# Optimization experiments

Measured on AMD Instinct MI355X. Metric: run time of the kernel, lower is better.

Reference implementation:

```python
import jax, jax.numpy as jnp
import numpy as np

CAP_FACTOR = 1.25


def _moe_top1(x, wg, w1, b1, w2, b2):
    """Top-1 switch MoE with capacity-based token dropping.
    x: [T, d]; wg: [d, E]; w1: [E, d, f]; b1: [E, f]; w2: [E, f, d]; b2: [E, d].
    """
    T, d = x.shape
    E = wg.shape[1]
    cap = int(CAP_FACTOR * T / E)
    probs = jax.nn.softmax(x @ wg, axis=-1)            # [T, E]
    idx = jnp.argmax(probs, axis=-1)                   # [T] expert assignment
    gate = jnp.max(probs, axis=-1)                     # [T] gate prob
    oh = jax.nn.one_hot(idx, E, dtype=jnp.int32)       # [T, E]
    # position of each token within its expert's buffer
    pos = (jnp.cumsum(oh, axis=0) * oh).sum(-1) - 1    # [T]
    keep = pos < cap                                   # drop tokens over capacity
    pos_w = jnp.where(keep, pos, cap)                  # dropped -> overflow slot
    # dispatch: scatter tokens into per-expert buffers [E, cap+1, d]
    buf = jnp.zeros((E, cap + 1, d), dtype=x.dtype).at[idx, pos_w].set(x)
    buf = buf[:, :cap]                                 # slice off overflow slot
    # grouped expert FFN
    h = jax.nn.relu(jnp.einsum('ecd,edf->ecf', buf, w1) + b1[:, None, :])
    eo = jnp.einsum('ecf,efd->ecd', h, w2) + b2[:, None, :]
    # combine: gather each token's expert output, scale by gate prob, zero dropped
    pos_g = jnp.minimum(pos_w, cap - 1)
    out = eo[idx, pos_g] * (gate * keep.astype(x.dtype))[:, None]
    return out


def setup_inputs():
    key = jax.random.key(0)
    ks = jax.random.split(key, 12)
    B, S, d, dff, E1, E2 = 8, 2048, 1024, 4096, 8, 16
    s = lambda fan: np.float32(1.0 / np.sqrt(fan))
    return dict(
        x=jax.random.normal(ks[0], (B, S, d), jnp.float32),
        y=jax.random.randint(ks[1], (B,), 0, d),
        wg1=jax.random.normal(ks[2], (d, E1), jnp.float32) * s(d),
        w1a=jax.random.normal(ks[3], (E1, d, dff), jnp.float32) * s(d),
        b1a=jnp.zeros((E1, dff), jnp.float32),
        w2a=jax.random.normal(ks[4], (E1, dff, d), jnp.float32) * s(dff),
        b2a=jnp.zeros((E1, d), jnp.float32),
        wg2=jax.random.normal(ks[5], (d, E2), jnp.float32) * s(d),
        w1b=jax.random.normal(ks[6], (E2, d, dff), jnp.float32) * s(d),
        b1b=jnp.zeros((E2, dff), jnp.float32),
        w2b=jax.random.normal(ks[7], (E2, dff, d), jnp.float32) * s(dff),
        b2b=jnp.zeros((E2, d), jnp.float32),
    )


def reference(x, y, wg1, w1a, b1a, w2a, b2a, wg2, w1b, b1b, w2b, b2b):
    B, S, d = x.shape
    xf = x.reshape(B * S, d)
    m1 = _moe_top1(xf, wg1, w1a, b1a, w2a, b2a)        # moe1(x)
    m2 = _moe_top1(m1, wg2, w1b, b1b, w2b, b2b)        # moe2(moe_out)
    resid = x + m2.reshape(B, S, d)                    # residual add
    sent = resid.mean(axis=1)                          # [B, d] mean-pool -> logits
    logp = jax.nn.log_softmax(sent, axis=-1)
    return -logp[jnp.arange(B), y].mean()              # cross-entropy loss
```

## Files before the change

### kernel.cpp

```cpp
#include <hip/hip_runtime.h>
#include <hip/hip_bf16.h>
#include <cstdint>
#include <cstddef>

#define B_    8
#define S_    2048
#define D_    1024
#define DFF_  4096
#define E1_   8
#define E2_   16
#define T_    (B_*S_)
#define CAP1_ 2560
#define CAP2_ 1280
#define EC_   20480

typedef __bf16 bf16x8 __attribute__((ext_vector_type(8)));
typedef float  f32x4  __attribute__((ext_vector_type(4)));

__device__ __forceinline__ unsigned short f2bf(float x) {
  return __builtin_bit_cast(unsigned short, (__bf16)x);
}

template<int E>
__global__ __launch_bounds__(256)
void gate_kernel(const float* __restrict__ X, const float* __restrict__ WG,
                 int* __restrict__ idxO, float* __restrict__ gateO) {
  const int lane = threadIdx.x & 63;
  const int wv   = threadIdx.x >> 6;
  const int t    = blockIdx.x * 4 + wv;
  const float* xr = X + (size_t)t * D_;
  float acc[E];
#pragma unroll
  for (int e = 0; e < E; ++e) acc[e] = 0.f;
#pragma unroll
  for (int i = 0; i < 4; ++i) {
    float4 xv = *(const float4*)(xr + i * 256 + lane * 4);
    int kb = i * 256 + lane * 4;
#pragma unroll
    for (int j = 0; j < 4; ++j) {
      float xs = (&xv.x)[j];
      const float* wr = WG + (size_t)(kb + j) * E;
#pragma unroll
      for (int e = 0; e < E; ++e) acc[e] += xs * wr[e];
    }
  }
#pragma unroll
  for (int e = 0; e < E; ++e) {
    float v = acc[e];
#pragma unroll
    for (int s = 32; s >= 1; s >>= 1) v += __shfl_xor(v, s, 64);
    acc[e] = v;
  }
  if (lane == 0) {
    float mx = acc[0]; int mi = 0;
#pragma unroll
    for (int e = 1; e < E; ++e) if (acc[e] > mx) { mx = acc[e]; mi = e; }
    float s = 0.f;
#pragma unroll
    for (int e = 0; e < E; ++e) s += expf(acc[e] - mx);
    idxO[t]  = mi;
    gateO[t] = 1.0f / s;
  }
}

__global__ __launch_bounds__(1024)
void scan_kernel(const int* __restrict__ idx, int E, int cap,
                 int* __restrict__ pos, int* __restrict__ kept) {
  __shared__ int cnt[16][17];
  __shared__ int gbase[16];
  const int tid = threadIdx.x;
  const int w = tid >> 6, lane = tid & 63;
  if (tid < E) gbase[tid] = 0;
  __syncthreads();
  const unsigned long long lt = (lane == 63) ? 0xFFFFFFFFFFFFFFFFull >> 1
                                             : ((1ull << lane) - 1ull);
  for (int it = 0; it < T_ / 1024; ++it) {
    int t = it * 1024 + tid;
    int mi = idx[t];
    int rank = 0;
    for (int e = 0; e < E; ++e) {
      unsigned long long m = __ballot(mi == e);
      if (lane == 0) cnt[w][e] = __popcll(m);
      if (mi == e) rank = __popcll(m & lt);
    }
    __syncthreads();
    int off = 0;
    for (int w2 = 0; w2 < w; ++w2) off += cnt[w2][mi];
    pos[t] = gbase[mi] + off + rank;
    __syncthreads();
    if (tid < E) {
      int tot = 0;
      for (int w2 = 0; w2 < 16; ++w2) tot += cnt[w2][tid];
      gbase[tid] += tot;
    }
    __syncthreads();
  }
  if (tid < E) kept[tid] = min(gbase[tid], cap);
}

__global__ __launch_bounds__(64)
void scatter_kernel(const float* __restrict__ X, const int* __restrict__ idx,
                    const int* __restrict__ pos, int cap,
                    unsigned short* __restrict__ xbuf, int* __restrict__ tokmap,
                    float* __restrict__ mzero) {
  const int t = blockIdx.x;
  const int lane = threadIdx.x;
  const int p = pos[t];
  if (p < cap) {
    const size_t dst = ((size_t)idx[t] * cap + p) * D_;
    const float* xr = X + (size_t)t * D_;
#pragma unroll
    for (int i = 0; i < 4; ++i) {
      float4 v = *(const float4*)(xr + i * 256 + lane * 4);
      ushort4 o;
      o.x = f2bf(v.x); o.y = f2bf(v.y); o.z = f2bf(v.z); o.w = f2bf(v.w);
      *(ushort4*)(xbuf + dst + i * 256 + lane * 4) = o;
    }
    if (lane == 0) tokmap[(size_t)idx[t] * cap + p] = t;
  } else {
    float4 z = {0.f, 0.f, 0.f, 0.f};
    float* mr = mzero + (size_t)t * D_;
#pragma unroll
    for (int i = 0; i < 4; ++i) *(float4*)(mr + i * 256 + lane * 4) = z;
  }
}

__global__ __launch_bounds__(256)
void wtrans_kernel(const float* __restrict__ src, unsigned short* __restrict__ dst,
                   int K, int N) {
  __shared__ float t[64][65];
  const int tid = threadIdx.x;
  const size_t eo = (size_t)blockIdx.z * K * N;
  const int k0 = blockIdx.y * 64, n0 = blockIdx.x * 64;
  const float* s = src + eo + (size_t)k0 * N + n0;
  unsigned short* d = dst + eo + (size_t)n0 * K + k0;
#pragma unroll
  for (int i = 0; i < 4; ++i) {
    int k = i * 16 + (tid >> 4);
    int n4 = (tid & 15) * 4;
    float4 v = *(const float4*)(s + (size_t)k * N + n4);
    t[k][n4] = v.x; t[k][n4 + 1] = v.y; t[k][n4 + 2] = v.z; t[k][n4 + 3] = v.w;
  }
  __syncthreads();
#pragma unroll
  for (int i = 0; i < 4; ++i) {
    int n = i * 16 + (tid >> 4);
    int k4 = (tid & 15) * 4;
    ushort4 o;
    o.x = f2bf(t[k4][n]);     o.y = f2bf(t[k4 + 1][n]);
    o.z = f2bf(t[k4 + 2][n]); o.w = f2bf(t[k4 + 3][n]);
    *(ushort4*)(d + (size_t)n * K + k4) = o;
  }
}

#define STG(BASEPTR, H, KT, SLOT) do {                                          \
    const unsigned short* _s = (BASEPTR) + (size_t)((H) * 128) * K + (KT) + st_off; \
    __builtin_amdgcn_global_load_lds((const __attribute__((address_space(1))) void*)_s, \
        (__attribute__((address_space(3))) void*)(smem + (SLOT) + dst0), 16, 0, 0);   \
    __builtin_amdgcn_global_load_lds((const __attribute__((address_space(1))) void*)(_s + (size_t)64 * K), \
        (__attribute__((address_space(3))) void*)(smem + (SLOT) + 8192 + dst0), 16, 0, 0); \
  } while (0)

#define RDA(BUF, MH) do { _Pragma("unroll")                                     \
    for (int m_ = 0; m_ < 4; ++m_) {                                            \
      const char* _p = smem + (BUF) * 65536 + aslot + ((MH) * 4 + m_) * 2048;   \
      af[m_][0] = *(const bf16x8*)(_p + va);                                    \
      af[m_][1] = *(const bf16x8*)(_p + (va ^ 64)); } } while (0)

#define RDB01(BUF, DEST) do { _Pragma("unroll")                                 \
    for (int j_ = 0; j_ < 2; ++j_) {                                            \
      const char* _p = smem + (BUF) * 65536 + bslot + j_ * 2048;                \
      DEST[j_][0] = *(const bf16x8*)(_p + vb);                                  \
      DEST[j_][1] = *(const bf16x8*)(_p + (vb ^ 64)); } } while (0)

#define RDB23(BUF) do { _Pragma("unroll")                                       \
    for (int j_ = 0; j_ < 2; ++j_) {                                            \
      const char* _p = smem + (BUF) * 65536 + bslot + (2 + j_) * 2048;          \
      bfb[j_][0] = *(const bf16x8*)(_p + vb);                                   \
      bfb[j_][1] = *(const bf16x8*)(_p + (vb ^ 64)); } } while (0)

#define QUADN0(MH, BA) do {                                                     \
    __builtin_amdgcn_s_setprio(1);                                              \
    _Pragma("unroll") for (int m_ = 0; m_ < 4; ++m_)                            \
    _Pragma("unroll") for (int j_ = 0; j_ < 2; ++j_)                            \
    _Pragma("unroll") for (int k_ = 0; k_ < 2; ++k_)                            \
      acc[(MH) * 4 + m_][j_] = __builtin_amdgcn_mfma_f32_16x16x32_bf16(         \
          af[m_][k_], BA[j_][k_], acc[(MH) * 4 + m_][j_], 0, 0, 0);             \
    __builtin_amdgcn_s_setprio(0);                                              \
  } while (0)

#define QUADN1(MH) do {                                                         \
    __builtin_amdgcn_s_setprio(1);                                              \
    _Pragma("unroll") for (int m_ = 0; m_ < 4; ++m_)                            \
    _Pragma("unroll") for (int j_ = 0; j_ < 2; ++j_)                            \
    _Pragma("unroll") for (int k_ = 0; k_ < 2; ++k_)                            \
      acc[(MH) * 4 + m_][2 + j_] = __builtin_amdgcn_mfma_f32_16x16x32_bf16(     \
          af[m_][k_], bfb[j_][k_], acc[(MH) * 4 + m_][2 + j_], 0, 0, 0);        \
    __builtin_amdgcn_s_setprio(0);                                              \
  } while (0)

#define SB0   __builtin_amdgcn_sched_barrier(0)
#define BAR   __builtin_amdgcn_s_barrier()
#define VM6   do { asm volatile("s_waitcnt vmcnt(6)" ::: "memory"); SB0; } while (0)
#define VM8   do { asm volatile("s_waitcnt vmcnt(8)" ::: "memory"); SB0; } while (0)
#define VM0   do { asm volatile("s_waitcnt vmcnt(0)" ::: "memory"); SB0; } while (0)

template<int MODE>
__global__ __launch_bounds__(512, 2)
void moe_gemm(const unsigned short* __restrict__ A,
              const unsigned short* __restrict__ BT,
              const float* __restrict__ bias, int K, int N, int cap, int nbcnt,
              const int* __restrict__ kept,
              unsigned short* __restrict__ Hout, float* __restrict__ Mout,
              const int* __restrict__ tokmap, const float* __restrict__ gate) {
  __shared__ char smem[131072];
  const int tid  = threadIdx.x;
  const int lane = tid & 63;
  const int wv   = tid >> 6;
  const int wr   = wv >> 2;
  const int wc   = wv & 3;

  const int nwg = gridDim.x;
  const int wg  = (blockIdx.x & 7) * (nwg >> 3) + (blockIdx.x >> 3);
  const int per_grp = nbcnt * 4;
  const int grp = wg / per_grp;
  const int rem = wg - grp * per_grp;
  const int mb  = grp * 4 + (rem & 3);
  const int nb  = rem >> 2;

  const int e  = (mb * 256) / cap;
  const int r0 = mb * 256 - e * cap;
  const int kept_e = kept[e];
  if (r0 >= kept_e) return;
  const unsigned short* Ab = A + (size_t)(mb * 256) * K;
  const unsigned short* Bb = BT + ((size_t)e * N + (size_t)nb * 256) * K;

  f32x4 acc[8][4];
#pragma unroll
  for (int m = 0; m < 8; ++m)
#pragma unroll
    for (int n = 0; n < 4; ++n) acc[m][n] = (f32x4){0.f, 0.f, 0.f, 0.f};

  const int scol   = ((tid & 7) ^ ((tid >> 3) & 7)) * 8;
  const size_t st_off = (size_t)(tid >> 3) * K + scol;
  const int dst0   = tid * 16;

  const int r16 = lane & 15;
  const int g16 = (lane >> 4) * 16;
  const int swz = (r16 & 7) * 16;
  const int va  = r16 * 128 + (g16 ^ swz);
  const int vb  = (wc & 1) * 8192 + va;
  const int aslot = wr * 16384;
  const int bslot = 32768 + (wc >> 1) * 16384;
  bf16x8 af[4][2], bA0[2][2], bA1[2][2], bfb[2][2];


  STG(Ab, 0, 0, 0);
  STG(Bb, 0, 0, 32768);
  STG(Bb, 1, 0, 49152);
  STG(Ab, 1, 0, 16384);
  STG(Ab, 0, 64, 65536);
  STG(Bb, 0, 64, 98304);
  STG(Bb, 1, 64, 114688);
  STG(Ab, 1, 64, 81920);
  VM8; BAR;
  RDB01(0, bA0);

  const int NT = K >> 6;
  const int NI = K >> 7;
  for (int i = 0; i < NI; ++i) {
    const bool last = (i == NI - 1);
    const bool s2 = (2 * i + 2) < NT;
    const bool s3 = (2 * i + 3) < NT;
    const int kt1 = (2 * i + 1) << 6;
    const int kt2 = (2 * i + 2) << 6;
    const int kt3 = (2 * i + 3) << 6;

    RDA(0, 0);
    if (i > 0) STG(Ab, 1, kt1, 81920);
    BAR; QUADN0(0, bA0); BAR;
    RDB23(0);
    if (s2) STG(Ab, 0, kt2, 0);
    BAR; QUADN1(0); BAR;
    RDA(0, 1);
    if (s2) STG(Bb, 0, kt2, 32768);
    BAR; QUADN1(1); BAR;
    if (s2) STG(Bb, 1, kt2, 49152);
    if (last) { VM0; } else { VM6; }
    RDB01(1, bA1);
    BAR; QUADN0(1, bA0); BAR;
    RDA(1, 0);
    if (s2) STG(Ab, 1, kt2, 16384);
    BAR; QUADN0(0, bA1); BAR;
    RDB23(1);
    if (s3) STG(Ab, 0, kt3, 65536);
    BAR; QUADN1(0); BAR;
    RDA(1, 1);
    if (s3) STG(Bb, 0, kt3, 98304);
    BAR; QUADN1(1); BAR;
    if (s3) STG(Bb, 1, kt3, 114688);
    if (!last) { VM6; RDB01(0, bA0); }
    BAR; QUADN0(1, bA1); BAR;
  }

  const int rg = lane >> 4;
  float bv[4];
#pragma unroll
  for (int n = 0; n < 4; ++n)
    bv[n] = bias[(size_t)e * N + nb * 256 + wc * 64 + n * 16 + r16];

#pragma unroll
  for (int m = 0; m < 8; ++m) {
#pragma unroll
    for (int r = 0; r < 4; ++r) {
      const int lrow = wr * 128 + m * 16 + rg * 4 + r;
      if (MODE == 0) {
        unsigned short* orow = Hout + (size_t)(mb * 256 + lrow) * N + nb * 256;
#pragma unroll
        for (int n = 0; n < 4; ++n) {
          float v = acc[m][n][r] + bv[n];
          orow[wc * 64 + n * 16 + r16] = f2bf(fmaxf(v, 0.f));
        }
      } else {
        const int lr = r0 + lrow;
        if (lr < kept_e) {
          const int tok = tokmap[mb * 256 + lrow];
          const float gsc = gate[tok];
          float* orow = Mout + (size_t)tok * N + nb * 256;
#pragma unroll
          for (int n = 0; n < 4; ++n)
            orow[wc * 64 + n * 16 + r16] = (acc[m][n][r] + bv[n]) * gsc;
        }
      }
    }
  }
}

__global__ __launch_bounds__(256)
void reduce_kernel(const float* __restrict__ X, const float* __restrict__ M2,
                   float* __restrict__ sent) {
  const int c = blockIdx.x * 256 + threadIdx.x;
  const int b = blockIdx.z;
  const int s0 = blockIdx.y * 128;
  float a = 0.f;
  size_t base = ((size_t)b * S_ + s0) * D_ + c;
  for (int s = 0; s < 128; ++s) a += X[base + (size_t)s * D_] + M2[base + (size_t)s * D_];
  atomicAdd(&sent[b * D_ + c], a * (1.0f / (float)S_));
}

__global__ __launch_bounds__(64)
void loss_kernel(const float* __restrict__ sent, const int* __restrict__ y,
                 float* __restrict__ out) {
  const int lane = threadIdx.x;
  float total = 0.f;
  for (int b = 0; b < B_; ++b) {
    const float* s = sent + b * D_;
    float v[16];
    float mx = -1e30f;
#pragma unroll
    for (int i = 0; i < 16; ++i) { v[i] = s[lane + i * 64]; mx = fmaxf(mx, v[i]); }
#pragma unroll
    for (int sh = 32; sh >= 1; sh >>= 1) mx = fmaxf(mx, __shfl_xor(mx, sh, 64));
    float sm = 0.f;
#pragma unroll
    for (int i = 0; i < 16; ++i) sm += expf(v[i] - mx);
#pragma unroll
    for (int sh = 32; sh >= 1; sh >>= 1) sm += __shfl_xor(sm, sh, 64);
    total += logf(sm) + mx - s[y[b]];
  }
  if (lane == 0) out[0] = total * (1.0f / (float)B_);
}

extern "C" void kernel_launch(void* const* d_in, const int* in_sizes, int n_in,
                              void* d_out, int out_size, void* d_ws, size_t ws_size,
                              hipStream_t stream) {
  const float* x   = (const float*)d_in[0];
  const int*   y   = (const int*)d_in[1];
  const float* wg1 = (const float*)d_in[2];
  const float* w1a = (const float*)d_in[3];
  const float* b1a = (const float*)d_in[4];
  const float* w2a = (const float*)d_in[5];
  const float* b2a = (const float*)d_in[6];
  const float* wg2 = (const float*)d_in[7];
  const float* w1b = (const float*)d_in[8];
  const float* b1b = (const float*)d_in[9];
  const float* w2b = (const float*)d_in[10];
  const float* b2b = (const float*)d_in[11];
  float* out = (float*)d_out;
  (void)in_sizes; (void)n_in; (void)out_size; (void)ws_size;

  char* base = (char*)d_ws;
  size_t o = 0;
  auto alloc = [&](size_t bytes) { size_t r = o; o = (o + bytes + 255) & ~(size_t)255; return r; };
  int*   idx1    = (int*)  (base + alloc((size_t)T_ * 4));
  int*   pos1    = (int*)  (base + alloc((size_t)T_ * 4));
  float* gate1   = (float*)(base + alloc((size_t)T_ * 4));
  int*   idx2    = (int*)  (base + alloc((size_t)T_ * 4));
  int*   pos2    = (int*)  (base + alloc((size_t)T_ * 4));
  float* gate2   = (float*)(base + alloc((size_t)T_ * 4));
  int*   kept1   = (int*)  (base + alloc(64 * 4));
  int*   kept2   = (int*)  (base + alloc(64 * 4));
  int*   tokmap1 = (int*)  (base + alloc((size_t)EC_ * 4));
  int*   tokmap2 = (int*)  (base + alloc((size_t)EC_ * 4));
  float* sent    = (float*)(base + alloc((size_t)B_ * D_ * 4));
  float* m1      = (float*)(base + alloc((size_t)T_ * D_ * 4));
  unsigned short* xbuf = (unsigned short*)(base + alloc((size_t)EC_ * D_ * 2));
  unsigned short* h    = (unsigned short*)(base + alloc((size_t)EC_ * DFF_ * 2));
  unsigned short* wT   = (unsigned short*)(base + alloc((size_t)E2_ * D_ * DFF_ * 2));

  hipMemsetAsync(sent, 0, (size_t)B_ * D_ * 4, stream);

  gate_kernel<E1_><<<T_ / 4, 256, 0, stream>>>(x, wg1, idx1, gate1);
  scan_kernel<<<1, 1024, 0, stream>>>(idx1, E1_, CAP1_, pos1, kept1);
  scatter_kernel<<<T_, 64, 0, stream>>>(x, idx1, pos1, CAP1_, xbuf, tokmap1, m1);
  wtrans_kernel<<<dim3(DFF_ / 64, D_ / 64, E1_), 256, 0, stream>>>(w1a, wT, D_, DFF_);
  moe_gemm<0><<<(DFF_ / 256) * (EC_ / 256), 512, 0, stream>>>(
      xbuf, wT, b1a, D_, DFF_, CAP1_, DFF_ / 256, kept1, h, nullptr, nullptr, nullptr);
  wtrans_kernel<<<dim3(D_ / 64, DFF_ / 64, E1_), 256, 0, stream>>>(w2a, wT, DFF_, D_);
  moe_gemm<1><<<(D_ / 256) * (EC_ / 256), 512, 0, stream>>>(
      h, wT, b2a, DFF_, D_, CAP1_, D_ / 256, kept1, nullptr, m1, tokmap1, gate1);

  gate_kernel<E2_><<<T_ / 4, 256, 0, stream>>>(m1, wg2, idx2, gate2);
  scan_kernel<<<1, 1024, 0, stream>>>(idx2, E2_, CAP2_, pos2, kept2);
  scatter_kernel<<<T_, 64, 0, stream>>>(m1, idx2, pos2, CAP2_, xbuf, tokmap2, m1);
  wtrans_kernel<<<dim3(DFF_ / 64, D_ / 64, E2_), 256, 0, stream>>>(w1b, wT, D_, DFF_);
  moe_gemm<0><<<(DFF_ / 256) * (EC_ / 256), 512, 0, stream>>>(
      xbuf, wT, b1b, D_, DFF_, CAP2_, DFF_ / 256, kept2, h, nullptr, nullptr, nullptr);
  wtrans_kernel<<<dim3(D_ / 64, DFF_ / 64, E2_), 256, 0, stream>>>(w2b, wT, DFF_, D_);
  moe_gemm<1><<<(D_ / 256) * (EC_ / 256), 512, 0, stream>>>(
      h, wT, b2b, DFF_, D_, CAP2_, D_ / 256, kept2, nullptr, m1, tokmap2, gate2);

  reduce_kernel<<<dim3(D_ / 256, S_ / 128, B_), 256, 0, stream>>>(x, m1, sent);
  loss_kernel<<<1, 64, 0, stream>>>(sent, y, out);
}
```

Baseline: 1.293 ms.

## Split-K the second expert GEMM with atomic accumulation into output

The down-projection GEMM (K=4096, N=1024) launches only 320 tiles, which may underfill the GPU. The K dimension is split in half so twice as many workgroups run, and each half atomically adds its gated partial result into the output. The scatter kernel now zeroes every output row, including kept tokens, so the atomic adds start from zero. In exchange this adds atomic traffic, extra zeroing writes, and a nondeterministic float summation order.

Measured after the change: 1.426 ms. 1.1x slower.

```diff
diff --git a/kernel.cpp b/kernel.cpp
--- a/kernel.cpp
+++ b/kernel.cpp
@@ -106,20 +106,21 @@
   const int t = blockIdx.x;
   const int lane = threadIdx.x;
   const int p = pos[t];
+  const float* xr = X + (size_t)t * D_;
+  float* mr = mzero + (size_t)t * D_;
+  const float4 z = {0.f, 0.f, 0.f, 0.f};
   if (p < cap) {
     const size_t dst = ((size_t)idx[t] * cap + p) * D_;
-    const float* xr = X + (size_t)t * D_;
 #pragma unroll
     for (int i = 0; i < 4; ++i) {
       float4 v = *(const float4*)(xr + i * 256 + lane * 4);
       ushort4 o;
       o.x = f2bf(v.x); o.y = f2bf(v.y); o.z = f2bf(v.z); o.w = f2bf(v.w);
       *(ushort4*)(xbuf + dst + i * 256 + lane * 4) = o;
+      *(float4*)(mr + i * 256 + lane * 4) = z;
     }
     if (lane == 0) tokmap[(size_t)idx[t] * cap + p] = t;
   } else {
-    float4 z = {0.f, 0.f, 0.f, 0.f};
-    float* mr = mzero + (size_t)t * D_;
 #pragma unroll
     for (int i = 0; i < 4; ++i) *(float4*)(mr + i * 256 + lane * 4) = z;
   }
@@ -209,7 +210,8 @@
 __global__ __launch_bounds__(512, 2)
 void moe_gemm(const unsigned short* __restrict__ A,
               const unsigned short* __restrict__ BT,
-              const float* __restrict__ bias, int K, int N, int cap, int nbcnt,
+              const float* __restrict__ bias, int K, int Kloop, int N, int cap,
+              int nbcnt, int ntiles,
               const int* __restrict__ kept,
               unsigned short* __restrict__ Hout, float* __restrict__ Mout,
               const int* __restrict__ tokmap, const float* __restrict__ gate) {
@@ -220,8 +222,12 @@
   const int wr   = wv >> 2;
   const int wc   = wv & 3;
 
-  const int nwg = gridDim.x;
-  const int wg  = (blockIdx.x & 7) * (nwg >> 3) + (blockIdx.x >> 3);
+  const int bid   = blockIdx.x;
+  const int khalf = (bid >= ntiles) ? 1 : 0;
+  const int lbid  = bid - khalf * ntiles;
+  const int koff  = khalf * Kloop;
+  const bool split = (Kloop != K);
+  const int wg  = (lbid & 7) * (ntiles >> 3) + (lbid >> 3);
   const int per_grp = nbcnt * 4;
   const int grp = wg / per_grp;
   const int rem = wg - grp * per_grp;
@@ -232,8 +238,8 @@
   const int r0 = mb * 256 - e * cap;
   const int kept_e = kept[e];
   if (r0 >= kept_e) return;
-  const unsigned short* Ab = A + (size_t)(mb * 256) * K;
-  const unsigned short* Bb = BT + ((size_t)e * N + (size_t)nb * 256) * K;
+  const unsigned short* Ab = A + (size_t)(mb * 256) * K + koff;
+  const unsigned short* Bb = BT + ((size_t)e * N + (size_t)nb * 256) * K + koff;
 
   f32x4 acc[8][4];
 #pragma unroll
@@ -266,8 +272,8 @@
   VM8; BAR;
   RDB01(0, bA0);
 
-  const int NT = K >> 6;
-  const int NI = K >> 7;
+  const int NT = Kloop >> 6;
+  const int NI = Kloop >> 7;
   for (int i = 0; i < NI; ++i) {
     const bool last = (i == NI - 1);
     const bool s2 = (2 * i + 2) < NT;
@@ -327,9 +333,17 @@
           const int tok = tokmap[mb * 256 + lrow];
           const float gsc = gate[tok];
           float* orow = Mout + (size_t)tok * N + nb * 256;
-#pragma unroll
-          for (int n = 0; n < 4; ++n)
-            orow[wc * 64 + n * 16 + r16] = (acc[m][n][r] + bv[n]) * gsc;
+          if (split) {
+#pragma unroll
+            for (int n = 0; n < 4; ++n) {
+              float v = acc[m][n][r] + (koff == 0 ? bv[n] : 0.f);
+              atomicAdd(&orow[wc * 64 + n * 16 + r16], v * gsc);
+            }
+          } else {
+#pragma unroll
+            for (int n = 0; n < 4; ++n)
+              orow[wc * 64 + n * 16 + r16] = (acc[m][n][r] + bv[n]) * gsc;
+          }
         }
       }
     }
@@ -410,25 +424,28 @@
 
   hipMemsetAsync(sent, 0, (size_t)B_ * D_ * 4, stream);
 
+  const int NT0 = (DFF_ / 256) * (EC_ / 256);
+  const int NT1 = (D_  / 256) * (EC_ / 256);
+
   gate_kernel<E1_><<<T_ / 4, 256, 0, stream>>>(x, wg1, idx1, gate1);
   scan_kernel<<<1, 1024, 0, stream>>>(idx1, E1_, CAP1_, pos1, kept1);
   scatter_kernel<<<T_, 64, 0, stream>>>(x, idx1, pos1, CAP1_, xbuf, tokmap1, m1);
   wtrans_kernel<<<dim3(DFF_ / 64, D_ / 64, E1_), 256, 0, stream>>>(w1a, wT, D_, DFF_);
-  moe_gemm<0><<<(DFF_ / 256) * (EC_ / 256), 512, 0, stream>>>(
-      xbuf, wT, b1a, D_, DFF_, CAP1_, DFF_ / 256, kept1, h, nullptr, nullptr, nullptr);
+  moe_gemm<0><<<NT0, 512, 0, stream>>>(
+      xbuf, wT, b1a, D_, D_, DFF_, CAP1_, DFF_ / 256, NT0, kept1, h, nullptr, nullptr, nullptr);
   wtrans_kernel<<<dim3(D_ / 64, DFF_ / 64, E1_), 256, 0, stream>>>(w2a, wT, DFF_, D_);
-  moe_gemm<1><<<(D_ / 256) * (EC_ / 256), 512, 0, stream>>>(
-      h, wT, b2a, DFF_, D_, CAP1_, D_ / 256, kept1, nullptr, m1, tokmap1, gate1);
+  moe_gemm<1><<<NT1 * 2, 512, 0, stream>>>(
+      h, wT, b2a, DFF_, DFF_ / 2, D_, CAP1_, D_ / 256, NT1, kept1, nullptr, m1, tokmap1, gate1);
 
   gate_kernel<E2_><<<T_ / 4, 256, 0, stream>>>(m1, wg2, idx2, gate2);
   scan_kernel<<<1, 1024, 0, stream>>>(idx2, E2_, CAP2_, pos2, kept2);
   scatter_kernel<<<T_, 64, 0, stream>>>(m1, idx2, pos2, CAP2_, xbuf, tokmap2, m1);
   wtrans_kernel<<<dim3(DFF_ / 64, D_ / 64, E2_), 256, 0, stream>>>(w1b, wT, D_, DFF_);
-  moe_gemm<0><<<(DFF_ / 256) * (EC_ / 256), 512, 0, stream>>>(
-      xbuf, wT, b1b, D_, DFF_, CAP2_, DFF_ / 256, kept2, h, nullptr, nullptr, nullptr);
+  moe_gemm<0><<<NT0, 512, 0, stream>>>(
+      xbuf, wT, b1b, D_, D_, DFF_, CAP2_, DFF_ / 256, NT0, kept2, h, nullptr, nullptr, nullptr);
   wtrans_kernel<<<dim3(D_ / 64, DFF_ / 64, E2_), 256, 0, stream>>>(w2b, wT, DFF_, D_);
-  moe_gemm<1><<<(D_ / 256) * (EC_ / 256), 512, 0, stream>>>(
-      h, wT, b2b, DFF_, D_, CAP2_, D_ / 256, kept2, nullptr, m1, tokmap2, gate2);
+  moe_gemm<1><<<NT1 * 2, 512, 0, stream>>>(
+      h, wT, b2b, DFF_, DFF_ / 2, D_, CAP2_, D_ / 256, NT1, kept2, nullptr, m1, tokmap2, gate2);
 
   reduce_kernel<<<dim3(D_ / 256, S_ / 128, B_), 256, 0, stream>>>(x, m1, sent);
   loss_kernel<<<1, 64, 0, stream>>>(sent, y, out);
```

## Switch expert GEMMs from bf16 to fp8 MFMA with fp8 activations and weights

Applied to the files above, without the earlier changes.

Converts the dispatched activations, transposed weights and hidden activations to fp8 (e4m3 via cvt_pk_fp8) and uses 16x16x32 fp8 MFMA in the grouped expert GEMMs. K-tiles double to 128 elements so each LDS slot keeps the same byte footprint, and the LDS read swizzle is reworked for 8-byte fragments. This halves memory traffic and uses the higher-throughput fp8 matrix path, at the cost of much lower precision in both FFN layers, which can change the loss. The hidden-layer epilogue now writes single bytes, which scatters the stores.

After: 1.309 ms. Within noise of the previous version (+1.2%).

```diff
diff --git a/kernel.cpp b/kernel.cpp
--- a/kernel.cpp
+++ b/kernel.cpp
@@ -14,11 +14,12 @@
 #define CAP2_ 1280
 #define EC_   20480
 
-typedef __bf16 bf16x8 __attribute__((ext_vector_type(8)));
-typedef float  f32x4  __attribute__((ext_vector_type(4)));
-
-__device__ __forceinline__ unsigned short f2bf(float x) {
-  return __builtin_bit_cast(unsigned short, (__bf16)x);
+typedef float f32x4 __attribute__((ext_vector_type(4)));
+
+__device__ __forceinline__ unsigned int pk4fp8(float a, float b, float c, float d) {
+  int r = __builtin_amdgcn_cvt_pk_fp8_f32(a, b, 0, false);
+  r = __builtin_amdgcn_cvt_pk_fp8_f32(c, d, r, true);
+  return (unsigned int)r;
 }
 
 template<int E>
@@ -101,7 +102,7 @@
 __global__ __launch_bounds__(64)
 void scatter_kernel(const float* __restrict__ X, const int* __restrict__ idx,
                     const int* __restrict__ pos, int cap,
-                    unsigned short* __restrict__ xbuf, int* __restrict__ tokmap,
+                    unsigned char* __restrict__ xbuf, int* __restrict__ tokmap,
                     float* __restrict__ mzero) {
   const int t = blockIdx.x;
   const int lane = threadIdx.x;
@@ -112,9 +113,7 @@
 #pragma unroll
     for (int i = 0; i < 4; ++i) {
       float4 v = *(const float4*)(xr + i * 256 + lane * 4);
-      ushort4 o;
-      o.x = f2bf(v.x); o.y = f2bf(v.y); o.z = f2bf(v.z); o.w = f2bf(v.w);
-      *(ushort4*)(xbuf + dst + i * 256 + lane * 4) = o;
+      *(unsigned int*)(xbuf + dst + i * 256 + lane * 4) = pk4fp8(v.x, v.y, v.z, v.w);
     }
     if (lane == 0) tokmap[(size_t)idx[t] * cap + p] = t;
   } else {
@@ -126,14 +125,14 @@
 }
 
 __global__ __launch_bounds__(256)
-void wtrans_kernel(const float* __restrict__ src, unsigned short* __restrict__ dst,
+void wtrans_kernel(const float* __restrict__ src, unsigned char* __restrict__ dst,
                    int K, int N) {
   __shared__ float t[64][65];
   const int tid = threadIdx.x;
   const size_t eo = (size_t)blockIdx.z * K * N;
   const int k0 = blockIdx.y * 64, n0 = blockIdx.x * 64;
   const float* s = src + eo + (size_t)k0 * N + n0;
-  unsigned short* d = dst + eo + (size_t)n0 * K + k0;
+  unsigned char* d = dst + eo + (size_t)n0 * K + k0;
 #pragma unroll
   for (int i = 0; i < 4; ++i) {
     int k = i * 16 + (tid >> 4);
@@ -146,15 +145,13 @@
   for (int i = 0; i < 4; ++i) {
     int n = i * 16 + (tid >> 4);
     int k4 = (tid & 15) * 4;
-    ushort4 o;
-    o.x = f2bf(t[k4][n]);     o.y = f2bf(t[k4 + 1][n]);
-    o.z = f2bf(t[k4 + 2][n]); o.w = f2bf(t[k4 + 3][n]);
-    *(ushort4*)(d + (size_t)n * K + k4) = o;
+    *(unsigned int*)(d + (size_t)n * K + k4) =
+        pk4fp8(t[k4][n], t[k4 + 1][n], t[k4 + 2][n], t[k4 + 3][n]);
   }
 }
 
 #define STG(BASEPTR, H, KT, SLOT) do {                                          \
-    const unsigned short* _s = (BASEPTR) + (size_t)((H) * 128) * K + (KT) + st_off; \
+    const unsigned char* _s = (BASEPTR) + (size_t)((H) * 128) * K + (KT) + st_off; \
     __builtin_amdgcn_global_load_lds((const __attribute__((address_space(1))) void*)_s, \
         (__attribute__((address_space(3))) void*)(smem + (SLOT) + dst0), 16, 0, 0);   \
     __builtin_amdgcn_global_load_lds((const __attribute__((address_space(1))) void*)(_s + (size_t)64 * K), \
@@ -163,28 +160,28 @@
 
 #define RDA(BUF, MH) do { _Pragma("unroll")                                     \
     for (int m_ = 0; m_ < 4; ++m_) {                                            \
-      const char* _p = smem + (BUF) * 65536 + aslot + ((MH) * 4 + m_) * 2048;   \
-      af[m_][0] = *(const bf16x8*)(_p + va);                                    \
-      af[m_][1] = *(const bf16x8*)(_p + (va ^ 64)); } } while (0)
+      const char* _p = smem + (BUF) * 65536 + aslot + ((MH) * 4 + m_) * 2048 + vaf; \
+      _Pragma("unroll") for (int k_ = 0; k_ < 4; ++k_)                          \
+        af[m_][k_] = *(const long long*)(_p + (((2 * k_ + c0) ^ swz7) << 4)); } } while (0)
 
 #define RDB01(BUF, DEST) do { _Pragma("unroll")                                 \
     for (int j_ = 0; j_ < 2; ++j_) {                                            \
-      const char* _p = smem + (BUF) * 65536 + bslot + j_ * 2048;                \
-      DEST[j_][0] = *(const bf16x8*)(_p + vb);                                  \
-      DEST[j_][1] = *(const bf16x8*)(_p + (vb ^ 64)); } } while (0)
+      const char* _p = smem + (BUF) * 65536 + bslot + j_ * 2048 + vbf;          \
+      _Pragma("unroll") for (int k_ = 0; k_ < 4; ++k_)                          \
+        DEST[j_][k_] = *(const long long*)(_p + (((2 * k_ + c0) ^ swz7) << 4)); } } while (0)
 
 #define RDB23(BUF) do { _Pragma("unroll")                                       \
     for (int j_ = 0; j_ < 2; ++j_) {                                            \
-      const char* _p = smem + (BUF) * 65536 + bslot + (2 + j_) * 2048;          \
-      bfb[j_][0] = *(const bf16x8*)(_p + vb);                                   \
-      bfb[j_][1] = *(const bf16x8*)(_p + (vb ^ 64)); } } while (0)
+      const char* _p = smem + (BUF) * 65536 + bslot + (2 + j_) * 2048 + vbf;    \
+      _Pragma("unroll") for (int k_ = 0; k_ < 4; ++k_)                          \
+        bfb[j_][k_] = *(const long long*)(_p + (((2 * k_ + c0) ^ swz7) << 4)); } } while (0)
 
 #define QUADN0(MH, BA) do {                                                     \
     __builtin_amdgcn_s_setprio(1);                                              \
     _Pragma("unroll") for (int m_ = 0; m_ < 4; ++m_)                            \
     _Pragma("unroll") for (int j_ = 0; j_ < 2; ++j_)                            \
-    _Pragma("unroll") for (int k_ = 0; k_ < 2; ++k_)                            \
-      acc[(MH) * 4 + m_][j_] = __builtin_amdgcn_mfma_f32_16x16x32_bf16(         \
+    _Pragma("unroll") for (int k_ = 0; k_ < 4; ++k_)                            \
+      acc[(MH) * 4 + m_][j_] = __builtin_amdgcn_mfma_f32_16x16x32_fp8_fp8(      \
           af[m_][k_], BA[j_][k_], acc[(MH) * 4 + m_][j_], 0, 0, 0);             \
     __builtin_amdgcn_s_setprio(0);                                              \
   } while (0)
@@ -193,8 +190,8 @@
     __builtin_amdgcn_s_setprio(1);                                              \
     _Pragma("unroll") for (int m_ = 0; m_ < 4; ++m_)                            \
     _Pragma("unroll") for (int j_ = 0; j_ < 2; ++j_)                            \
-    _Pragma("unroll") for (int k_ = 0; k_ < 2; ++k_)                            \
-      acc[(MH) * 4 + m_][2 + j_] = __builtin_amdgcn_mfma_f32_16x16x32_bf16(     \
+    _Pragma("unroll") for (int k_ = 0; k_ < 4; ++k_)                            \
+      acc[(MH) * 4 + m_][2 + j_] = __builtin_amdgcn_mfma_f32_16x16x32_fp8_fp8(  \
           af[m_][k_], bfb[j_][k_], acc[(MH) * 4 + m_][2 + j_], 0, 0, 0);        \
     __builtin_amdgcn_s_setprio(0);                                              \
   } while (0)
@@ -207,11 +204,11 @@
 
 template<int MODE>
 __global__ __launch_bounds__(512, 2)
-void moe_gemm(const unsigned short* __restrict__ A,
-              const unsigned short* __restrict__ BT,
+void moe_gemm(const unsigned char* __restrict__ A,
+              const unsigned char* __restrict__ BT,
               const float* __restrict__ bias, int K, int N, int cap, int nbcnt,
               const int* __restrict__ kept,
-              unsigned short* __restrict__ Hout, float* __restrict__ Mout,
+              unsigned char* __restrict__ Hout, float* __restrict__ Mout,
               const int* __restrict__ tokmap, const float* __restrict__ gate) {
   __shared__ char smem[131072];
   const int tid  = threadIdx.x;
@@ -232,8 +229,8 @@
   const int r0 = mb * 256 - e * cap;
   const int kept_e = kept[e];
   if (r0 >= kept_e) return;
-  const unsigned short* Ab = A + (size_t)(mb * 256) * K;
-  const unsigned short* Bb = BT + ((size_t)e * N + (size_t)nb * 256) * K;
+  const unsigned char* Ab = A + (size_t)(mb * 256) * K;
+  const unsigned char* Bb = BT + ((size_t)e * N + (size_t)nb * 256) * K;
 
   f32x4 acc[8][4];
 #pragma unroll
@@ -241,40 +238,40 @@
 #pragma unroll
     for (int n = 0; n < 4; ++n) acc[m][n] = (f32x4){0.f, 0.f, 0.f, 0.f};
 
-  const int scol   = ((tid & 7) ^ ((tid >> 3) & 7)) * 8;
+  const int scol   = ((tid & 7) ^ ((tid >> 3) & 7)) * 16;
   const size_t st_off = (size_t)(tid >> 3) * K + scol;
   const int dst0   = tid * 16;
 
-  const int r16 = lane & 15;
-  const int g16 = (lane >> 4) * 16;
-  const int swz = (r16 & 7) * 16;
-  const int va  = r16 * 128 + (g16 ^ swz);
-  const int vb  = (wc & 1) * 8192 + va;
+  const int r16  = lane & 15;
+  const int l34  = lane >> 4;
+  const int c0   = l34 >> 1;
+  const int swz7 = r16 & 7;
+  const int vaf  = r16 * 128 + (l34 & 1) * 8;
+  const int vbf  = (wc & 1) * 8192 + vaf;
   const int aslot = wr * 16384;
   const int bslot = 32768 + (wc >> 1) * 16384;
-  bf16x8 af[4][2], bA0[2][2], bA1[2][2], bfb[2][2];
-
+  long long af[4][4], bA0[2][4], bA1[2][4], bfb[2][4];
 
   STG(Ab, 0, 0, 0);
   STG(Bb, 0, 0, 32768);
   STG(Bb, 1, 0, 49152);
   STG(Ab, 1, 0, 16384);
-  STG(Ab, 0, 64, 65536);
-  STG(Bb, 0, 64, 98304);
-  STG(Bb, 1, 64, 114688);
-  STG(Ab, 1, 64, 81920);
+  STG(Ab, 0, 128, 65536);
+  STG(Bb, 0, 128, 98304);
+  STG(Bb, 1, 128, 114688);
+  STG(Ab, 1, 128, 81920);
   VM8; BAR;
   RDB01(0, bA0);
 
-  const int NT = K >> 6;
-  const int NI = K >> 7;
+  const int NT = K >> 7;
+  const int NI = K >> 8;
   for (int i = 0; i < NI; ++i) {
     const bool last = (i == NI - 1);
     const bool s2 = (2 * i + 2) < NT;
     const bool s3 = (2 * i + 3) < NT;
-    const int kt1 = (2 * i + 1) << 6;
-    const int kt2 = (2 * i + 2) << 6;
-    const int kt3 = (2 * i + 3) << 6;
+    const int kt1 = (2 * i + 1) << 7;
+    const int kt2 = (2 * i + 2) << 7;
+    const int kt3 = (2 * i + 3) << 7;
 
     RDA(0, 0);
     if (i > 0) STG(Ab, 1, kt1, 81920);
@@ -315,12 +312,15 @@
     for (int r = 0; r < 4; ++r) {
       const int lrow = wr * 128 + m * 16 + rg * 4 + r;
       if (MODE == 0) {
-        unsigned short* orow = Hout + (size_t)(mb * 256 + lrow) * N + nb * 256;
-#pragma unroll
-        for (int n = 0; n < 4; ++n) {
-          float v = acc[m][n][r] + bv[n];
-          orow[wc * 64 + n * 16 + r16] = f2bf(fmaxf(v, 0.f));
-        }
+        unsigned char* orow = Hout + (size_t)(mb * 256 + lrow) * N + nb * 256;
+        unsigned int q = pk4fp8(fmaxf(acc[m][0][r] + bv[0], 0.f),
+                                fmaxf(acc[m][1][r] + bv[1], 0.f),
+                                fmaxf(acc[m][2][r] + bv[2], 0.f),
+                                fmaxf(acc[m][3][r] + bv[3], 0.f));
+        orow[wc * 64 +  0 + r16] = (unsigned char)(q & 0xff);
+        orow[wc * 64 + 16 + r16] = (unsigned char)((q >> 8) & 0xff);
+        orow[wc * 64 + 32 + r16] = (unsigned char)((q >> 16) & 0xff);
+        orow[wc * 64 + 48 + r16] = (unsigned char)(q >> 24);
       } else {
         const int lr = r0 + lrow;
         if (lr < kept_e) {
@@ -404,9 +404,9 @@
   int*   tokmap2 = (int*)  (base + alloc((size_t)EC_ * 4));
   float* sent    = (float*)(base + alloc((size_t)B_ * D_ * 4));
   float* m1      = (float*)(base + alloc((size_t)T_ * D_ * 4));
-  unsigned short* xbuf = (unsigned short*)(base + alloc((size_t)EC_ * D_ * 2));
-  unsigned short* h    = (unsigned short*)(base + alloc((size_t)EC_ * DFF_ * 2));
-  unsigned short* wT   = (unsigned short*)(base + alloc((size_t)E2_ * D_ * DFF_ * 2));
+  unsigned char* xbuf = (unsigned char*)(base + alloc((size_t)EC_ * D_));
+  unsigned char* h    = (unsigned char*)(base + alloc((size_t)EC_ * DFF_));
+  unsigned char* wT   = (unsigned char*)(base + alloc((size_t)E2_ * D_ * DFF_));
 
   hipMemsetAsync(sent, 0, (size_t)B_ * D_ * 4, stream);
 
```
